# Optimization experiments

Measured on AMD Instinct MI355X. Metric: run time of the kernel, lower is better.

Reference implementation:

```python
import jax, jax.numpy as jnp
import numpy as np

# ---- config (mirrors init_kwargs) ----
H = 128
W = 128
FMO_STEPS = 4
INPUT_FRAMES = 1
N_PIECES = 1
N_TERMS = 2
CAM_DIST = 2.0
ROT_DIVIDE = 1.0
SIGMAINV = 7000.0
ERODE_K = 5
FOCAL = float(1.0 / np.tan(1.57 / 4.0))  # generate_perspective_projection(1.57/2), aspect=1


def quaternion_to_angle_axis(q):
    # q: [B,4] in (w,x,y,z) convention (torchgeometry)
    q1, q2, q3 = q[..., 1], q[..., 2], q[..., 3]
    sin_sq = q1 * q1 + q2 * q2 + q3 * q3
    sin_t = jnp.sqrt(sin_sq + 1e-20)
    cos_t = q[..., 0]
    two_theta = 2.0 * jnp.where(cos_t < 0.0, jnp.arctan2(-sin_t, -cos_t), jnp.arctan2(sin_t, cos_t))
    k = jnp.where(sin_sq > 1e-12, two_theta / sin_t, 2.0)
    return q[..., 1:4] * k[..., None]


def angle_axis_to_rotation_matrix(aa):
    # aa: [B,3] -> [B,3,3] (Rodrigues)
    th = jnp.sqrt(jnp.sum(aa * aa, axis=-1, keepdims=True) + 1e-12)  # [B,1]
    k = aa / th
    kx, ky, kz = k[..., 0], k[..., 1], k[..., 2]
    zero = jnp.zeros_like(kx)
    K = jnp.stack([jnp.stack([zero, -kz, ky], -1),
                   jnp.stack([kz, zero, -kx], -1),
                   jnp.stack([-ky, kx, zero], -1)], -2)
    s = jnp.sin(th)[..., None]
    c = jnp.cos(th)[..., None]
    return jnp.eye(3, dtype=aa.dtype) + s * K + (1.0 - c) * jnp.matmul(K, K)


def rasterize(fv_img, fv_z, face_feat, fn_z):
    # fv_img [B,F,3,2] NDC, fv_z [B,F,3] camera z, face_feat [B,F,3,C], fn_z [B,F]
    B, F = fv_img.shape[:2]
    xs = jnp.linspace(-1.0, 1.0, W)
    ys = jnp.linspace(1.0, -1.0, H)
    py, px = jnp.meshgrid(ys, xs, indexing='ij')  # [H,W]
    a, b, c = fv_img[:, :, 0], fv_img[:, :, 1], fv_img[:, :, 2]  # [B,F,2]
    e0 = b - a
    e1 = c - a
    denom = e0[..., 0] * e1[..., 1] - e0[..., 1] * e1[..., 0]  # [B,F]
    valid = (fn_z > 0.0) & (jnp.abs(denom) > 1e-10)
    inv_den = jnp.where(jnp.abs(denom) > 1e-10, 1.0 / denom, 0.0)
    dx = px[None, None] - a[..., 0][..., None, None]  # [B,F,H,W]
    dy = py[None, None] - a[..., 1][..., None, None]
    w1 = (dx * e1[..., 1][..., None, None] - dy * e1[..., 0][..., None, None]) * inv_den[..., None, None]
    w2 = (e0[..., 0][..., None, None] * dy - e0[..., 1][..., None, None] * dx) * inv_den[..., None, None]
    w0 = 1.0 - w1 - w2
    inside = (w0 >= 0.0) & (w1 >= 0.0) & (w2 >= 0.0) & valid[..., None, None]
    zi = (w0 * fv_z[:, :, 0, None, None] + w1 * fv_z[:, :, 1, None, None] + w2 * fv_z[:, :, 2, None, None])
    score = jnp.where(inside, zi, -1e10)  # camera looks down -z: nearest face has max z
    best = jnp.argmax(score, axis=1)      # [B,H,W] z-buffer winner
    hit = jnp.any(inside, axis=1)
    bary = jnp.stack([w0, w1, w2], axis=-1)  # [B,F,H,W,3]
    idx = jnp.broadcast_to(best[:, None, :, :, None], (B, 1, H, W, 3))
    bary_b = jnp.take_along_axis(bary, idx, axis=1)[:, 0]  # [B,H,W,3]
    feat_b = jax.vmap(lambda f, i: f[i])(face_feat, best)  # [B,H,W,3,C]
    feats = jnp.einsum('bhwkc,bhwk->bhwc', feat_b, bary_b) * hit[..., None]
    # DIB-R soft silhouette: A = 1 - prod(1 - exp(-sigmainv*d^2)), d = dist to triangle, 0 inside
    d2 = None
    tri = (a, b, c)
    for i in range(3):
        p, q = tri[i], tri[(i + 1) % 3]
        ex = (q - p)[..., 0][..., None, None]
        ey = (q - p)[..., 1][..., None, None]
        rx = px[None, None] - p[..., 0][..., None, None]
        ry = py[None, None] - p[..., 1][..., None, None]
        L2 = ex * ex + ey * ey + 1e-12
        t = jnp.clip((rx * ex + ry * ey) / L2, 0.0, 1.0)
        dxe = rx - t * ex
        dye = ry - t * ey
        dd = dxe * dxe + dye * dye
        d2 = dd if d2 is None else jnp.minimum(d2, dd)
    d2 = jnp.where(inside, 0.0, d2)
    prob = jnp.where(valid[..., None, None], jnp.exp(-SIGMAINV * d2), 0.0)
    mask = 1.0 - jnp.prod(1.0 - prob, axis=1)  # [B,H,W]
    return feats, mask


def texture_sample(tex, uv):
    # tex [B,3,Th,Tw], uv [B,H,W,2] in [0,1]; bilinear, v axis flipped (image row 0 <-> v=1)
    Th, Tw = tex.shape[2], tex.shape[3]
    u = jnp.clip(uv[..., 0], 0.0, 1.0) * (Tw - 1)
    v = (1.0 - jnp.clip(uv[..., 1], 0.0, 1.0)) * (Th - 1)
    x0 = jnp.floor(u)
    y0 = jnp.floor(v)
    fx = (u - x0)[:, None]  # [B,1,H,W]
    fy = (v - y0)[:, None]
    x0i = jnp.clip(x0.astype(jnp.int32), 0, Tw - 1)
    x1i = jnp.clip(x0i + 1, 0, Tw - 1)
    y0i = jnp.clip(y0.astype(jnp.int32), 0, Th - 1)
    y1i = jnp.clip(y0i + 1, 0, Th - 1)
    g = jax.vmap(lambda t, yy, xx: t[:, yy, xx])  # [B,3,H,W]
    t00 = g(tex, y0i, x0i)
    t01 = g(tex, y0i, x1i)
    t10 = g(tex, y1i, x0i)
    t11 = g(tex, y1i, x1i)
    return t00 * (1 - fx) * (1 - fy) + t01 * fx * (1 - fy) + t10 * (1 - fx) * fy + t11 * fx * fy


def erode(m, k):
    # kornia erosion with an all-ones kxk kernel == min-pool (geodesic border)
    return -jax.lax.reduce_window(-m, -jnp.inf, jax.lax.max, (1, k, k), (1, 1, 1), 'SAME')


def render_frame(verts_world, faces, face_features, texture_maps):
    # camera at (0,0,CAM_DIST) looking at origin with up=(0,1,0): R_cam == I
    v_cam = verts_world - jnp.array([0.0, 0.0, CAM_DIST], dtype=verts_world.dtype)
    fv_cam = v_cam[:, faces]  # [B,F,3,3]
    n = jnp.cross(fv_cam[:, :, 1] - fv_cam[:, :, 0], fv_cam[:, :, 2] - fv_cam[:, :, 0])
    n = n / (jnp.linalg.norm(n, axis=-1, keepdims=True) + 1e-10)
    fn_z = n[..., 2]
    z = fv_cam[..., 2]  # negative in front of camera
    img = FOCAL * fv_cam[..., :2] / (-z[..., None] + 1e-10)  # [B,F,3,2]
    uv, mask = rasterize(img, z, face_features, fn_z)
    rgb = texture_sample(texture_maps, uv)  # [B,3,H,W]
    mask_e = erode(mask, ERODE_K)
    return jnp.concatenate([rgb, mask_e[:, None]], axis=1)  # [B,4,H,W]


def reference(vertices, translation, quaternion, exp, face_features, texture_maps, faces):
    rot = angle_axis_to_rotation_matrix(quaternion_to_angle_axis(quaternion[:, 0, 0]))
    trans_start = translation[:, :, 0, 0]  # [B,1,3]
    all_renders = []
    renders = []
    frames = 0
    time_before = 0.0
    for pind in range(N_PIECES):
        angles = quaternion_to_angle_axis(quaternion[:, pind, 1]) / ROT_DIVIDE
        rot_step = angle_axis_to_rotation_matrix(exp * angles / FMO_STEPS)
        rot_noexp = angle_axis_to_rotation_matrix(angles * (1.0 - exp))
        n_steps = FMO_STEPS * INPUT_FRAMES // N_PIECES  # prop[pind] (forced for single piece)
        for ti in np.linspace(0.0, 1.0, n_steps):
            if frames == 0:
                time_before = ti
            time_exp = time_before + (ti - time_before) * exp  # [1]
            verts = jnp.einsum('bij,bvj->bvi', rot, vertices) + trans_start
            for p in range(1, N_TERMS):
                verts = verts + (time_exp ** p) * translation[:, :, pind, p]
            renders.append(render_frame(verts, faces, face_features, texture_maps))
            frames += 1
            if frames == FMO_STEPS:
                frames = 0
                all_renders.append(jnp.stack(renders, 1))
                renders = []
                rot = jnp.matmul(rot, rot_noexp)
            else:
                rot = jnp.matmul(rot, rot_step)
        for p in range(1, N_TERMS):
            trans_start = trans_start + translation[:, :, pind, p]
    return jnp.stack(all_renders, 1)  # [B, input_frames, fmo_steps, 4, H, W]


def setup_inputs() -> dict:
    key = jax.random.key(0)
    ks = jax.random.split(key, 7)
    B, V, F = 1, 162, 320
    vertices = jax.random.normal(ks[0], (B, V, 3), jnp.float32) * 0.3
    translation = jax.random.normal(ks[1], (B, 1, N_PIECES, N_TERMS, 3), jnp.float32) * 0.1
    quaternion = jax.random.normal(ks[2], (B, N_PIECES, 2, 4), jnp.float32)
    exp = jax.random.uniform(ks[3], (1,), jnp.float32)
    face_features = jax.random.uniform(ks[4], (B, F, 3, 2), jnp.float32)
    texture_maps = jax.random.uniform(ks[5], (B, 3, 256, 256), jnp.float32)
    faces = jax.random.randint(ks[6], (F, 3), 0, V)
    return {"vertices": vertices, "translation": translation, "quaternion": quaternion,
            "exp": exp, "face_features": face_features, "texture_maps": texture_maps,
            "faces": faces}
```

## Files before the change

### kernel.cpp

```cpp
#include <hip/hip_runtime.h>
#include <math.h>

#define N_FRAMES 4
#define N_FACES  320
#define N_VERTS  162
#define IMG_H    128
#define IMG_W    128
#define NWAVES   8
#define FPW      40
#define REC_SZ   20

#define SV_OFF   0
#define BB_OFF   1952
#define BB_LD    48
#define REC_OFF  8096
#define ARENA_SZ 33696



__device__ __forceinline__ void q_to_aa(const float* q, float* aa) {
    float q1 = q[1], q2 = q[2], q3 = q[3];
    float sin_sq = (q1 * q1 + q2 * q2) + q3 * q3;
    float sin_t = sqrtf(sin_sq + 1e-20f);
    float cos_t = q[0];
    float two_theta = (cos_t < 0.0f) ? (2.0f * atan2f(-sin_t, -cos_t))
                                     : (2.0f * atan2f(sin_t, cos_t));
    float k = (sin_sq > 1e-12f) ? (two_theta / sin_t) : 2.0f;
    aa[0] = q1 * k; aa[1] = q2 * k; aa[2] = q3 * k;
}

__device__ __forceinline__ void aa_to_R(const float* aa, float* R) {
    float th = sqrtf(((aa[0] * aa[0] + aa[1] * aa[1]) + aa[2] * aa[2]) + 1e-12f);
    float kx = aa[0] / th, ky = aa[1] / th, kz = aa[2] / th;
    float K[9] = { 0.0f, -kz,  ky,
                   kz,  0.0f, -kx,
                  -ky,   kx, 0.0f };
    float s = sinf(th), c = cosf(th);
    float KK[9];
    for (int i = 0; i < 3; ++i)
        for (int j = 0; j < 3; ++j)
            KK[i*3+j] = (K[i*3+0] * K[0*3+j] + K[i*3+1] * K[1*3+j]) + K[i*3+2] * K[2*3+j];
    float omc = 1.0f - c;
    for (int i = 0; i < 9; ++i) {
        float eye = (i == 0 || i == 4 || i == 8) ? 1.0f : 0.0f;
        R[i] = (eye + s * K[i]) + omc * KK[i];
    }
}

__device__ __forceinline__ void mat3mul(const float* A, const float* B, float* C) {
    for (int i = 0; i < 3; ++i)
        for (int j = 0; j < 3; ++j)
            C[i*3+j] = (A[i*3+0] * B[0*3+j] + A[i*3+1] * B[1*3+j]) + A[i*3+2] * B[2*3+j];
}

__device__ __forceinline__ void halo_rc(int h, int* r, int* c) {
    if (h < 40)      { *r = h / 20;                *c = h % 20; }
    else if (h < 80) { int idx = h - 40; *r = 6 + idx / 20; *c = idx % 20; }
    else             { int s = h - 80; *r = 2 + (s >> 2);
                       int co = s & 3; *c = (co < 2) ? co : (16 + co); }
}

__device__ __forceinline__ float face_mask_factor(
    float px, float py,
    float ax, float ay, float e0x, float e0y, float e1x, float e1y,
    float invden, float invL2_0,
    float bx, float by, float e12x, float e12y,
    float cx, float cy, float invL2_1, float invL2_2)
{
    float dx = px - ax, dy = py - ay;
    float w1 = (dx * e1y - dy * e1x) * invden;
    float w2 = (e0x * dy - e0y * dx) * invden;
    float w0 = (1.0f - w1) - w2;
    bool inside = (w0 >= 0.0f) & (w1 >= 0.0f) & (w2 >= 0.0f);
    float t0 = fminf(fmaxf((dx * e0x + dy * e0y) * invL2_0, 0.0f), 1.0f);
    float x0 = dx - t0 * e0x, y0 = dy - t0 * e0y;
    float dd = x0 * x0 + y0 * y0;
    float rx1 = px - bx, ry1 = py - by;
    float t1 = fminf(fmaxf((rx1 * e12x + ry1 * e12y) * invL2_1, 0.0f), 1.0f);
    float x1 = rx1 - t1 * e12x, y1 = ry1 - t1 * e12y;
    dd = fminf(dd, x1 * x1 + y1 * y1);
    float ex2 = -e1x, ey2 = -e1y;
    float rx2 = px - cx, ry2 = py - cy;
    float t2 = fminf(fmaxf((rx2 * ex2 + ry2 * ey2) * invL2_2, 0.0f), 1.0f);
    float x2 = rx2 - t2 * ex2, y2 = ry2 - t2 * ey2;
    dd = fminf(dd, x2 * x2 + y2 * y2);
    float d2 = inside ? 0.0f : dd;
    float prob = __expf(-7000.0f * d2);
    return 1.0f - prob;
}


__global__ void __launch_bounds__(512)
render_kernel(const float* __restrict__ verts_in,
              const float* __restrict__ transl,
              const float* __restrict__ quat,
              const float* __restrict__ expv,
              const int*   __restrict__ faces,
              const float* __restrict__ ffeat,
              const float* __restrict__ tex,
              float* __restrict__ out)
{
    __shared__ __align__(16) char arena[ARENA_SZ];
    __shared__ float rotS[9];
    float* sv    = (float*)(arena + SV_OFF);
    float* bb    = (float*)(arena + BB_OFF);
    float* recs  = (float*)(arena + REC_OFF);
    float* red   = (float*)arena;
    float* hredp = (float*)(arena + 12288);
    float* m20   = (float*)(arena + 15360);

    int frame = blockIdx.x & 3;
    int blk   = blockIdx.x >> 2;
    int tid   = threadIdx.x;
    int lane  = tid & 63;
    int wv    = __builtin_amdgcn_readfirstlane(tid >> 6);
    int tile_x = blk & 7, tile_y = blk >> 3;
    int j = tile_x * 16 + (lane & 15);
    int i = tile_y * 4 + (lane >> 4);

    float e = expv[0];

    if (tid == 0) {
        float aa0[3], aa1[3], Rl[9], S[9];
        q_to_aa(quat, aa0);
        aa_to_R(aa0, Rl);
        q_to_aa(quat + 4, aa1);
        float arg[3];
        for (int t = 0; t < 3; ++t) arg[t] = (e * aa1[t]) / 4.0f;
        aa_to_R(arg, S);
        for (int t = 0; t < frame; ++t) {
            float nxt[9];
            mat3mul(Rl, S, nxt);
            for (int q = 0; q < 9; ++q) Rl[q] = nxt[q];
        }
        for (int q = 0; q < 9; ++q) rotS[q] = Rl[q];
    }
    __syncthreads();

    if (tid < N_VERTS) {
        float te = (float)((double)frame / 3.0) * e;
        float vx = verts_in[tid*3+0], vy = verts_in[tid*3+1], vz = verts_in[tid*3+2];
        float dx_ = (rotS[0] * vx + rotS[1] * vy) + rotS[2] * vz;
        float dy_ = (rotS[3] * vx + rotS[4] * vy) + rotS[5] * vz;
        float dz_ = (rotS[6] * vx + rotS[7] * vy) + rotS[8] * vz;
        float x = (dx_ + transl[0]) + te * transl[3];
        float y = (dy_ + transl[1]) + te * transl[4];
        float z = (dz_ + transl[2]) + te * transl[5];
        z = z - 2.0f;
        sv[tid*3+0] = x; sv[tid*3+1] = y; sv[tid*3+2] = z;
    }
    __syncthreads();

    const float FOCAL = (float)(1.0 / tan(1.57 / 4.0));
    int cnt;
    {
        bool valid = false;
        float ax=0, ay=0, bx=0, by=0, cx=0, cy=0, e0x=0, e0y=0, e1x=0, e1y=0;
        float e12x=0, e12y=0, z0=0, z1=0, z2=0, den=0;
        int f = wv * FPW + lane;
        if (lane < FPW) {
            int i0 = faces[f*3+0], i1 = faces[f*3+1], i2 = faces[f*3+2];
            const float* A = &sv[i0*3];
            const float* B = &sv[i1*3];
            const float* C = &sv[i2*3];
            float ux = B[0] - A[0], uy = B[1] - A[1];
            float wx = C[0] - A[0], wy = C[1] - A[1];
            float nz = ux * wy - uy * wx;
            float da = -A[2] + 1e-10f, db = -B[2] + 1e-10f, dc = -C[2] + 1e-10f;
            ax = (FOCAL * A[0]) / da; ay = (FOCAL * A[1]) / da;
            bx = (FOCAL * B[0]) / db; by = (FOCAL * B[1]) / db;
            cx = (FOCAL * C[0]) / dc; cy = (FOCAL * C[1]) / dc;
            e0x = bx - ax; e0y = by - ay;
            e1x = cx - ax; e1y = cy - ay;
            e12x = cx - bx; e12y = cy - by;
            den = e0x * e1y - e0y * e1x;
            z0 = A[2]; z1 = B[2]; z2 = C[2];
            valid = (fabsf(den) > 1e-10f) && (nz > 0.0f);
        }
        unsigned long long m = __ballot(valid);
        cnt = __popcll(m);
        if (valid) {
            unsigned long long lmask = (lane == 63) ? 0x7fffffffffffffffull
                                                    : ((1ull << lane) - 1ull);
            int pos = __popcll(m & lmask);
            float invden = 1.0f / den;
            float L2_0 = (e0x * e0x + e0y * e0y) + 1e-12f;
            float L2_1 = (e12x * e12x + e12y * e12y) + 1e-12f;
            float L2_2 = (e1x * e1x + e1y * e1y) + 1e-12f;
            float4* r = (float4*)&recs[(wv * FPW + pos) * REC_SZ];
            r[0] = make_float4(ax, ay, e0x, e0y);
            r[1] = make_float4(e1x, e1y, invden, (float)f);
            r[2] = make_float4(z0, z1, z2, 1.0f / L2_0);
            r[3] = make_float4(bx, by, e12x, e12y);
            r[4] = make_float4(cx, cy, 1.0f / L2_1, 1.0f / L2_2);
            float* wbb = &bb[wv * 4 * BB_LD];
            wbb[0*BB_LD + pos] = fminf(fminf(ax, bx), cx);
            wbb[1*BB_LD + pos] = fminf(fminf(ay, by), cy);
            wbb[2*BB_LD + pos] = fmaxf(fmaxf(ax, bx), cx);
            wbb[3*BB_LD + pos] = fmaxf(fmaxf(ay, by), cy);
        }
    }

    float px = (float)(-1.0 + 2.0 * (double)j / 127.0);
    float py = (float)( 1.0 - 2.0 * (double)i / 127.0);
    float txminH = (float)(-1.0 + 2.0 * (double)(tile_x * 16 - 2) / 127.0);
    float txmaxH = (float)(-1.0 + 2.0 * (double)(tile_x * 16 + 17) / 127.0);
    float tymaxH = (float)( 1.0 - 2.0 * (double)(tile_y * 4 - 2) / 127.0);
    float tyminH = (float)( 1.0 - 2.0 * (double)(tile_y * 4 + 5) / 127.0);

    float pxA, pyA, pxB = 0.0f, pyB = 0.0f;
    bool hasB = lane < 32;
    {
        int rA, cA; halo_rc(lane, &rA, &cA);
        int iA = tile_y * 4 + rA - 2, jA = tile_x * 16 + cA - 2;
        pxA = (float)(-1.0 + 2.0 * (double)jA / 127.0);
        pyA = (float)( 1.0 - 2.0 * (double)iA / 127.0);
        if (hasB) {
            int rB, cB; halo_rc(64 + lane, &rB, &cB);
            int iB = tile_y * 4 + rB - 2, jB = tile_x * 16 + cB - 2;
            pxB = (float)(-1.0 + 2.0 * (double)jB / 127.0);
            pyB = (float)( 1.0 - 2.0 * (double)iB / 127.0);
        }
    }

    unsigned long long fmask;
    {
        int l = (lane < FPW) ? lane : 0;
        const float* wbb = &bb[wv * 4 * BB_LD];
        float xmin = wbb[0*BB_LD + l], ymin = wbb[1*BB_LD + l];
        float xmax = wbb[2*BB_LD + l], ymax = wbb[3*BB_LD + l];
        float cdx = fmaxf(fmaxf(xmin - txmaxH, txminH - xmax), 0.0f);
        float cdy = fmaxf(fmaxf(ymin - tymaxH, tyminH - ymax), 0.0f);
        bool near = ((cdx * cdx + cdy * cdy) <= 0.0026f) && (lane < cnt);
        fmask = __ballot(near);
    }

    float best = -1e10f;
    int bestf = 0;
    float bw0 = 0.0f, bw1 = 0.0f, bw2 = 0.0f;
    float P = 1.0f;
    float PA = 1.0f, PB = hasB ? 1.0f : 0.0f;
    bool allzero = false;

    while (fmask) {
        int fc = __ffsll((unsigned long long)fmask) - 1;
        fmask &= fmask - 1;
        const float* d = &recs[(wv * FPW + fc) * REC_SZ];

        float ax = d[0], ay = d[1], e0x = d[2], e0y = d[3];
        float e1x = d[4], e1y = d[5], invden = d[6], fidx = d[7];
        float z0 = d[8], z1 = d[9], z2 = d[10];

        float dx = px - ax, dy = py - ay;
        float w1 = (dx * e1y - dy * e1x) * invden;
        float w2 = (e0x * dy - e0y * dx) * invden;
        float w0 = (1.0f - w1) - w2;
        bool inside = (w0 >= 0.0f) & (w1 >= 0.0f) & (w2 >= 0.0f);
        float zi = (w0 * z0 + w1 * z1) + w2 * z2;
        float score = inside ? zi : -1e10f;
        if (score > best) {
            best = score; bestf = (int)fidx; bw0 = w0; bw1 = w1; bw2 = w2;
        }

        if (!allzero) {
            float invL2_0 = d[11];
            float bx = d[12], by = d[13], e12x = d[14], e12y = d[15];
            float cx = d[16], cy = d[17], invL2_1 = d[18], invL2_2 = d[19];
            float t0 = fminf(fmaxf((dx * e0x + dy * e0y) * invL2_0, 0.0f), 1.0f);
            float x0 = dx - t0 * e0x, y0 = dy - t0 * e0y;
            float dd = x0 * x0 + y0 * y0;
            float rx1 = px - bx, ry1 = py - by;
            float t1 = fminf(fmaxf((rx1 * e12x + ry1 * e12y) * invL2_1, 0.0f), 1.0f);
            float x1 = rx1 - t1 * e12x, y1 = ry1 - t1 * e12y;
            dd = fminf(dd, x1 * x1 + y1 * y1);
            float ex2 = -e1x, ey2 = -e1y;
            float rx2 = px - cx, ry2 = py - cy;
            float t2 = fminf(fmaxf((rx2 * ex2 + ry2 * ey2) * invL2_2, 0.0f), 1.0f);
            float x2 = rx2 - t2 * ex2, y2 = ry2 - t2 * ey2;
            dd = fminf(dd, x2 * x2 + y2 * y2);

            float d2 = inside ? 0.0f : dd;
            float prob = __expf(-7000.0f * d2);
            P *= (1.0f - prob);

            PA *= face_mask_factor(pxA, pyA, ax, ay, e0x, e0y, e1x, e1y,
                                   invden, invL2_0, bx, by, e12x, e12y,
                                   cx, cy, invL2_1, invL2_2);
            if (hasB)
                PB *= face_mask_factor(pxB, pyB, ax, ay, e0x, e0y, e1x, e1y,
                                       invden, invL2_0, bx, by, e12x, e12y,
                                       cx, cy, invL2_1, invL2_2);

            allzero = __all((P == 0.0f) & (PA == 0.0f) & (PB == 0.0f));
        }
    }

    __syncthreads();
    float* my = &red[tid * 6];
    my[0] = best; my[1] = __int_as_float(bestf);
    my[2] = bw0;  my[3] = bw1; my[4] = bw2; my[5] = P;
    hredp[wv * 96 + lane] = PA;
    if (hasB) hredp[wv * 96 + 64 + lane] = PB;
    __syncthreads();

    if (tid < 64) {
        float bbst = red[tid * 6 + 0];
        int   bf   = __float_as_int(red[tid * 6 + 1]);
        float r0 = red[tid * 6 + 2], r1 = red[tid * 6 + 3], r2 = red[tid * 6 + 4];
        float Pt = red[tid * 6 + 5];
        for (int w = 1; w < NWAVES; ++w) {
            const float* s = &red[(w * 64 + tid) * 6];
            float sc = s[0]; int ff = __float_as_int(s[1]);
            if ((sc > bbst) || ((sc == bbst) && (ff < bf))) {
                bbst = sc; bf = ff; r0 = s[2]; r1 = s[3]; r2 = s[4];
            }
            Pt *= s[5];
        }

        bool hit = bbst != -1e10f;
        float uv0 = 0.0f, uv1 = 0.0f;
        if (hit) {
            const float* fp = ffeat + bf * 6;
            uv0 = (fp[0] * r0 + fp[2] * r1) + fp[4] * r2;
            uv1 = (fp[1] * r0 + fp[3] * r1) + fp[5] * r2;
        }
        float u = fminf(fmaxf(uv0, 0.0f), 1.0f) * 255.0f;
        float v = (1.0f - fminf(fmaxf(uv1, 0.0f), 1.0f)) * 255.0f;
        float x0f = floorf(u), y0f = floorf(v);
        float fx = u - x0f, fy = v - y0f;
        int x0i = min(max((int)x0f, 0), 255);
        int x1i = min(x0i + 1, 255);
        int y0i = min(max((int)y0f, 0), 255);
        int y1i = min(y0i + 1, 255);

        for (int c = 0; c < 3; ++c) {
            const float* tc = tex + c * 65536;
            float t00 = tc[y0i * 256 + x0i];
            float t01 = tc[y0i * 256 + x1i];
            float t10 = tc[y1i * 256 + x0i];
            float t11 = tc[y1i * 256 + x1i];
            float val = (t00 * (1.0f - fx)) * (1.0f - fy);
            val = val + (t01 * fx) * (1.0f - fy);
            val = val + (t10 * (1.0f - fx)) * fy;
            val = val + (t11 * fx) * fy;
            out[((frame * 4 + c) * IMG_H + i) * IMG_W + j] = val;
        }
        m20[(2 + (tid >> 4)) * 20 + (2 + (tid & 15))] = 1.0f - Pt;
    } else if (tid < 160) {
        int h = tid - 64;
        float p = hredp[h];
        for (int w = 1; w < NWAVES; ++w) p *= hredp[w * 96 + h];
        int r, c; halo_rc(h, &r, &c);
        int ii = tile_y * 4 + r - 2, jj = tile_x * 16 + c - 2;
        bool inimg = (ii >= 0) && (ii < IMG_H) && (jj >= 0) && (jj < IMG_W);
        m20[r * 20 + c] = inimg ? (1.0f - p) : 1e30f;
    }
    __syncthreads();

    if (tid < 64) {
        int r = 2 + (tid >> 4), c = 2 + (tid & 15);
        float mn = 1e30f;
        for (int dr = -2; dr <= 2; ++dr)
            for (int dc = -2; dc <= 2; ++dc)
                mn = fminf(mn, m20[(r + dr) * 20 + (c + dc)]);
        out[((frame * 4 + 3) * IMG_H + i) * IMG_W + j] = mn;
    }
}


extern "C" void kernel_launch(void* const* d_in, const int* in_sizes, int n_in,
                              void* d_out, int out_size, void* d_ws, size_t ws_size,
                              hipStream_t stream) {
    const float* vertices      = (const float*)d_in[0];
    const float* translation   = (const float*)d_in[1];
    const float* quaternion    = (const float*)d_in[2];
    const float* expv          = (const float*)d_in[3];
    const float* face_features = (const float*)d_in[4];
    const float* texture_maps  = (const float*)d_in[5];
    const int*   faces         = (const int*)d_in[6];
    float* out = (float*)d_out;
    (void)d_ws; (void)ws_size;

    render_kernel<<<N_FRAMES * 256, 512, 0, stream>>>(vertices, translation,
                                                      quaternion, expv, faces,
                                                      face_features, texture_maps,
                                                      out);
}
```

Before: 90.36 us.

## Balance near-face work evenly across waves using shared per-wave masks

Each wave now publishes its ballot mask of faces near the tile to shared memory, and all waves then split the total near-face list evenly instead of each handling only its own 40 faces. This targets load imbalance, where one wave with many nearby faces sets the block's runtime. It adds a block barrier, a shared-mask read of eight 64-bit values and a small prefix walk to find each wave's start. The per-wave partial results still rely on the existing cross-wave reduction afterward.

```diff
diff --git a/kernel.cpp b/kernel.cpp
--- a/kernel.cpp
+++ b/kernel.cpp
@@ -102,6 +102,7 @@
 {
     __shared__ __align__(16) char arena[ARENA_SZ];
     __shared__ float rotS[9];
+    __shared__ unsigned long long wmaskS[NWAVES];
     float* sv    = (float*)(arena + SV_OFF);
     float* bb    = (float*)(arena + BB_OFF);
     float* recs  = (float*)(arena + REC_OFF);
@@ -151,8 +152,14 @@
     }
     __syncthreads();
 
+    float px = (float)(-1.0 + 2.0 * (double)j / 127.0);
+    float py = (float)( 1.0 - 2.0 * (double)i / 127.0);
+    float txminH = (float)(-1.0 + 2.0 * (double)(tile_x * 16 - 2) / 127.0);
+    float txmaxH = (float)(-1.0 + 2.0 * (double)(tile_x * 16 + 17) / 127.0);
+    float tymaxH = (float)( 1.0 - 2.0 * (double)(tile_y * 4 - 2) / 127.0);
+    float tyminH = (float)( 1.0 - 2.0 * (double)(tile_y * 4 + 5) / 127.0);
+
     const float FOCAL = (float)(1.0 / tan(1.57 / 4.0));
-    int cnt;
     {
         bool valid = false;
         float ax=0, ay=0, bx=0, by=0, cx=0, cy=0, e0x=0, e0y=0, e1x=0, e1y=0;
@@ -178,7 +185,7 @@
             valid = (fabsf(den) > 1e-10f) && (nz > 0.0f);
         }
         unsigned long long m = __ballot(valid);
-        cnt = __popcll(m);
+        int cnt = __popcll(m);
         if (valid) {
             unsigned long long lmask = (lane == 63) ? 0x7fffffffffffffffull
                                                     : ((1ull << lane) - 1ull);
@@ -199,14 +206,17 @@
             wbb[2*BB_LD + pos] = fmaxf(fmaxf(ax, bx), cx);
             wbb[3*BB_LD + pos] = fmaxf(fmaxf(ay, by), cy);
         }
-    }
-
-    float px = (float)(-1.0 + 2.0 * (double)j / 127.0);
-    float py = (float)( 1.0 - 2.0 * (double)i / 127.0);
-    float txminH = (float)(-1.0 + 2.0 * (double)(tile_x * 16 - 2) / 127.0);
-    float txmaxH = (float)(-1.0 + 2.0 * (double)(tile_x * 16 + 17) / 127.0);
-    float tymaxH = (float)( 1.0 - 2.0 * (double)(tile_y * 4 - 2) / 127.0);
-    float tyminH = (float)( 1.0 - 2.0 * (double)(tile_y * 4 + 5) / 127.0);
+        int l = (lane < FPW) ? lane : 0;
+        const float* wbb = &bb[wv * 4 * BB_LD];
+        float xmin = wbb[0*BB_LD + l], ymin = wbb[1*BB_LD + l];
+        float xmax = wbb[2*BB_LD + l], ymax = wbb[3*BB_LD + l];
+        float cdx = fmaxf(fmaxf(xmin - txmaxH, txminH - xmax), 0.0f);
+        float cdy = fmaxf(fmaxf(ymin - tymaxH, tyminH - ymax), 0.0f);
+        bool near = ((cdx * cdx + cdy * cdy) <= 0.0026f) && (lane < cnt);
+        unsigned long long fm = __ballot(near);
+        if (lane == 0) wmaskS[wv] = fm;
+    }
+    __syncthreads();
 
     float pxA, pyA, pxB = 0.0f, pyB = 0.0f;
     bool hasB = lane < 32;
@@ -223,16 +233,24 @@
         }
     }
 
-    unsigned long long fmask;
-    {
-        int l = (lane < FPW) ? lane : 0;
-        const float* wbb = &bb[wv * 4 * BB_LD];
-        float xmin = wbb[0*BB_LD + l], ymin = wbb[1*BB_LD + l];
-        float xmax = wbb[2*BB_LD + l], ymax = wbb[3*BB_LD + l];
-        float cdx = fmaxf(fmaxf(xmin - txmaxH, txminH - xmax), 0.0f);
-        float cdy = fmaxf(fmaxf(ymin - tymaxH, tyminH - ymax), 0.0f);
-        bool near = ((cdx * cdx + cdy * cdy) <= 0.0026f) && (lane < cnt);
-        fmask = __ballot(near);
+    unsigned long long wm[NWAVES];
+    int R = 0;
+    #pragma unroll
+    for (int w = 0; w < NWAVES; ++w) { wm[w] = wmaskS[w]; R += __popcll(wm[w]); }
+    int q = R >> 3, rem = R & 7;
+    int start = wv * q + min(wv, rem);
+    int count = q + ((wv < rem) ? 1 : 0);
+
+    int seg = 0, csum = 0;
+    unsigned long long cur = 0;
+    if (count > 0) {
+        for (;;) {
+            int pc = __popcll(wm[seg]);
+            if (csum + pc > start) break;
+            csum += pc; ++seg;
+        }
+        cur = wm[seg];
+        for (int k = csum; k < start; ++k) cur &= cur - 1;
     }
 
     float best = -1e10f;
@@ -242,10 +260,11 @@
     float PA = 1.0f, PB = hasB ? 1.0f : 0.0f;
     bool allzero = false;
 
-    while (fmask) {
-        int fc = __ffsll((unsigned long long)fmask) - 1;
-        fmask &= fmask - 1;
-        const float* d = &recs[(wv * FPW + fc) * REC_SZ];
+    for (int n = 0; n < count; ++n) {
+        while (cur == 0ull) { ++seg; cur = wm[seg]; }
+        int fc = __ffsll((unsigned long long)cur) - 1;
+        cur &= cur - 1;
+        const float* d = &recs[(seg * FPW + fc) * REC_SZ];
 
         float ax = d[0], ay = d[1], e0x = d[2], e0y = d[3];
         float e1x = d[4], e1y = d[5], invden = d[6], fidx = d[7];
```

Measured after the change: 93.09 us. +3.0%, slower.
